# Kernel optimization log

Measured on AMD Instinct MI355X. Metric: run time of the kernel, lower is better.

Reference implementation:

```python
import jax, jax.numpy as jnp
import numpy as np
from jax import lax

GROUPS = 8
EPS = 1e-5


def _gconv(x, W, b, padding):
    y = lax.conv_general_dilated(
        x, W, window_strides=(1, 1), padding=padding,
        feature_group_count=GROUPS,
        dimension_numbers=("NCHW", "OIHW", "NCHW"))
    return y + b[None, :, None, None]


def setup_inputs() -> dict:
    key = jax.random.key(0)
    ks = jax.random.split(key, 9)
    B, C, H, Wd = 2, 256, 48, 48
    cpg = C // GROUPS  # 32 channels per group
    s3 = 1.0 / np.sqrt(cpg * 9)
    s1 = 1.0 / np.sqrt(cpg)
    return {
        "x": jax.random.normal(ks[0], (B, C, H, Wd), jnp.float32),
        "Wq": jax.random.normal(ks[1], (C, cpg, 3, 3), jnp.float32) * s3,
        "bq": jax.random.normal(ks[2], (C,), jnp.float32) * 0.01,
        "Wk": jax.random.normal(ks[3], (C, cpg, 1, 1), jnp.float32) * s1,
        "bk": jax.random.normal(ks[4], (C,), jnp.float32) * 0.01,
        "Wv": jax.random.normal(ks[5], (C, cpg, 1, 1), jnp.float32) * s1,
        "bv": jax.random.normal(ks[6], (C,), jnp.float32) * 0.01,
        "gamma": jnp.ones((C,), jnp.float32),
        "beta": jnp.zeros((C,), jnp.float32),
    }


def reference(x, Wq, bq, Wk, bk, Wv, bv, gamma, beta):
    b, c, h, w = x.shape
    g = GROUPS
    d = c // g  # head dim per group
    hw = h * w

    xq = _gconv(x, Wq, bq, "SAME")    # [b,c,h,w], 3x3 stride1 pad1
    xk = _gconv(x, Wk, bk, "VALID")   # 1x1
    xv = _gconv(x, Wv, bv, "VALID")   # 1x1

    q = xq.reshape(b, g, d, hw)  # k stays [b,g,d,hw]; q,v used as [b,g,hw,d]
    k = xk.reshape(b, g, d, hw)
    v = xv.reshape(b, g, d, hw)

    scale = jnp.asarray(d, x.dtype) ** -0.5
    attn = jnp.einsum("bgdn,bgdm->bgnm", q, k) * scale  # [b,g,hw,hw]
    attn = jax.nn.softmax(attn, axis=-1)
    out = jnp.einsum("bgnm,bgdm->bgdn", attn, v)  # [b,g,d,hw]
    out = out.reshape(b, c, h, w)

    # BatchNorm2d in training mode: biased batch stats over (N,H,W)
    mean = jnp.mean(out, axis=(0, 2, 3), keepdims=True)
    var = jnp.var(out, axis=(0, 2, 3), keepdims=True)
    out = (out - mean) * lax.rsqrt(var + EPS)
    out = out * gamma[None, :, None, None] + beta[None, :, None, None]
    return jax.nn.relu(out)
```

## Files before the change

### kernel.cpp

```cpp
#include <hip/hip_runtime.h>
#include <math.h>

#define BB 2
#define CC 256
#define GG 8
#define DD 32
#define HH 48
#define WW 48
#define HWSZ (HH*WW)
#define NHW (BB*HWSZ)
#define TOT (BB*CC*HWSZ)
#define NBG (BB*GG)
#define KSPLIT 4
#define KSEG (HWSZ/KSPLIT)
#define VTILE 2048
#define ATTN_SCALE (0.17677669529663687f * 1.4426950408889634f)

__device__ __align__(16) short g_q[NBG*HWSZ*DD];
__device__ __align__(16) short g_k[NBG*HWSZ*DD + 2048];
__device__ __align__(16) short g_v[NBG*DD*HWSZ + 2048];
__device__ __align__(16) float g_o[TOT];
__device__ __align__(16) short g_wq[GG*9*2*16*32];
__device__ __align__(16) short g_wk[CC*DD];
__device__ __align__(16) short g_wv[CC*DD];

typedef __attribute__((ext_vector_type(8))) short bf16x8;
typedef __attribute__((ext_vector_type(4))) short s16x4;
typedef __attribute__((ext_vector_type(4))) float f32x4;

__device__ __forceinline__ short f2bf(float f) {
    union { float f; unsigned u; } uf; uf.f = f;
    unsigned r = uf.u + 0x7fff + ((uf.u >> 16) & 1);
    return (short)(r >> 16);
}
__device__ __forceinline__ unsigned cvt_pk_bf16(float lo, float hi) {
    unsigned w;
    asm("v_cvt_pk_bf16_f32 %0, %1, %2" : "=v"(w) : "v"(lo), "v"(hi));
    return w;
}
#if __has_builtin(__builtin_amdgcn_exp2f)
#define EXP2F(x) __builtin_amdgcn_exp2f(x)
#else
#define EXP2F(x) exp2f(x)
#endif

__global__ __launch_bounds__(256) void pack_w(
    const float* __restrict__ Wq, const float* __restrict__ Wk,
    const float* __restrict__ Wv)
{
    int t = blockIdx.x * 256 + threadIdx.x;
    if (t < CC*DD*9) {
        int c = t / 288, r = t % 288, ci = r / 9, tap = r % 9;
        int g = c >> 5, mh = (c >> 4) & 1, l = c & 15;
        g_wq[(((g*9 + tap)*2 + mh)*16 + l)*32 + ci] = f2bf(Wq[t]);
    } else if (t < CC*DD*9 + CC*DD) {
        int i = t - CC*DD*9;
        g_wk[i] = f2bf(Wk[i]);
    } else if (t < CC*DD*9 + 2*CC*DD) {
        int i = t - CC*DD*9 - CC*DD;
        g_wv[i] = f2bf(Wv[i]);
    }
}

__global__ __launch_bounds__(256) void conv_mfma(
    const float* __restrict__ x,
    const float* __restrict__ bq, const float* __restrict__ bk,
    const float* __restrict__ bv)
{
    __shared__ __align__(16) short xt[4*48*40];

    int tid = threadIdx.x;
    int bg = blockIdx.x & 15;
    int pt = blockIdx.x >> 4;
    int p0 = pt * 64;
    int b = bg >> 3, g = bg & 7;
    int r0 = p0 / 48 - 1;
    const float* xb = x + ((size_t)(b*CC + g*DD)) * HWSZ;

    #pragma unroll 4
    for (int i = 0; i < 24; ++i) {
        int cell = tid + i * 256;
        int ci = cell / 192;
        int rc = cell % 192;
        int row = r0 + rc / 48, col = rc % 48;
        float v = (row >= 0 && row < 48) ? xb[(size_t)ci*HWSZ + row*48 + col] : 0.f;
        xt[rc*40 + ci] = f2bf(v);
    }
    __syncthreads();

    int lane = tid & 63, wave = tid >> 6;
    int l15 = lane & 15, lg = lane >> 4;

    bf16x8 aq[9][2], ak[2], av[2];
    const short* wqg = g_wq + g*9*2*16*32;
    #pragma unroll
    for (int tap = 0; tap < 9; ++tap)
        #pragma unroll
        for (int mh = 0; mh < 2; ++mh)
            aq[tap][mh] = *(const bf16x8*)&wqg[((tap*2 + mh)*16 + l15)*32 + lg*8];
    #pragma unroll
    for (int mh = 0; mh < 2; ++mh) {
        ak[mh] = *(const bf16x8*)&g_wk[(g*32 + mh*16 + l15)*32 + lg*8];
        av[mh] = *(const bf16x8*)&g_wv[(g*32 + mh*16 + l15)*32 + lg*8];
    }
    float bqv[2][4], bkv[2][4], bvv[2][4];
    #pragma unroll
    for (int mh = 0; mh < 2; ++mh)
        #pragma unroll
        for (int j = 0; j < 4; ++j) {
            int c = g*32 + mh*16 + lg*4 + j;
            bqv[mh][j] = bq[c]; bkv[mh][j] = bk[c]; bvv[mh][j] = bv[c];
        }

    size_t qkb = (size_t)bg * HWSZ * DD;
    size_t vb  = (size_t)bg * DD * HWSZ;
    const f32x4 zero = {0.f,0.f,0.f,0.f};

    int n = p0 + wave * 16 + l15;
    int y = n / 48, xcol = n % 48;
    int cell = (y - r0) * 48 + xcol;
    f32x4 cq0 = zero, cq1 = zero, ck0 = zero, ck1 = zero, cv0 = zero, cv1 = zero;
    #pragma unroll
    for (int tap = 0; tap < 9; ++tap) {
        int dy = tap / 3 - 1, dx = tap % 3 - 1;
        int xc = xcol + dx;
        bool ok = (unsigned)xc < 48u;
        int idx = ok ? (cell + dy*48 + dx)*40 + lg*8 : lg*8;
        bf16x8 bx = *(const bf16x8*)&xt[idx];
        if (!ok) bx = bf16x8{0,0,0,0,0,0,0,0};
        cq0 = __builtin_amdgcn_mfma_f32_16x16x32_bf16(aq[tap][0], bx, cq0, 0, 0, 0);
        cq1 = __builtin_amdgcn_mfma_f32_16x16x32_bf16(aq[tap][1], bx, cq1, 0, 0, 0);
        if (tap == 4) {
            ck0 = __builtin_amdgcn_mfma_f32_16x16x32_bf16(ak[0], bx, ck0, 0, 0, 0);
            ck1 = __builtin_amdgcn_mfma_f32_16x16x32_bf16(ak[1], bx, ck1, 0, 0, 0);
            cv0 = __builtin_amdgcn_mfma_f32_16x16x32_bf16(av[0], bx, cv0, 0, 0, 0);
            cv1 = __builtin_amdgcn_mfma_f32_16x16x32_bf16(av[1], bx, cv1, 0, 0, 0);
        }
    }
    int tile = n >> 6, key = n & 63;
    #pragma unroll
    for (int mh = 0; mh < 2; ++mh) {
        f32x4 aQ = mh ? cq1 : cq0;
        f32x4 aK = mh ? ck1 : ck0;
        f32x4 aV = mh ? cv1 : cv0;
        s16x4 pq, pk;
        #pragma unroll
        for (int j = 0; j < 4; ++j) {
            pq[j] = f2bf((aQ[j] + bqv[mh][j]) * ATTN_SCALE);
            pk[j] = f2bf(aK[j] + bkv[mh][j]);
        }
        *(s16x4*)&g_q[qkb + (size_t)n*32 + mh*16 + lg*4] = pq;
        *(s16x4*)&g_k[qkb + (size_t)n*32 + mh*16 + lg*4] = pk;
        #pragma unroll
        for (int j = 0; j < 4; ++j)
            g_v[vb + (size_t)tile*VTILE + (mh*16 + lg*4 + j)*64 + key]
                = f2bf(aV[j] + bvv[mh][j]);
    }
}

__global__ __launch_bounds__(256) void attn_mfma()
{
    __shared__ float cmb[KSPLIT][48][34];
    __shared__ float cmbl[KSPLIT][48];

    int tid  = threadIdx.x;
    int lane = tid & 63;
    int ks   = tid >> 6;
    int l15 = lane & 15;
    int lg  = lane >> 4;
    int bg = blockIdx.x & 15;
    int qt = blockIdx.x >> 4;

    const short* qg = g_q + (size_t)bg * HWSZ * DD;
    const short* kg = g_k + (size_t)bg * HWSZ * DD;
    const short* vg = g_v + (size_t)bg * DD * HWSZ;
    int k0 = ks * KSEG;

    bf16x8 aq0 = *(const bf16x8*)&qg[(size_t)(qt*48 + l15)*32 + lg*8];
    bf16x8 aq1 = *(const bf16x8*)&qg[(size_t)(qt*48 + 16 + l15)*32 + lg*8];
    bf16x8 aq2 = *(const bf16x8*)&qg[(size_t)(qt*48 + 32 + l15)*32 + lg*8];

    f32x4 oc00 = {0.f,0.f,0.f,0.f}, oc01 = {0.f,0.f,0.f,0.f};
    f32x4 oc10 = {0.f,0.f,0.f,0.f}, oc11 = {0.f,0.f,0.f,0.f};
    f32x4 oc20 = {0.f,0.f,0.f,0.f}, oc21 = {0.f,0.f,0.f,0.f};
    const f32x4 zero = {0.f,0.f,0.f,0.f};
    float lsum0 = 0.f, lsum1 = 0.f, lsum2 = 0.f;

    int koff = l15*32 + lg*8;
    int voff = l15*64 + lg*8;

    const short* kp = kg + (size_t)k0 * 32;
    const short* vp = vg + (size_t)(ks*9) * VTILE;

    bf16x8 ck[4], cv[4];
    #pragma unroll
    for (int kb = 0; kb < 4; ++kb)
        ck[kb] = *(const bf16x8*)&kp[koff + kb*512];
    #pragma unroll
    for (int h = 0; h < 2; ++h)
        #pragma unroll
        for (int w = 0; w < 2; ++w)
            cv[h*2+w] = *(const bf16x8*)&vp[voff + w*1024 + h*32];

    const short* kq = kp + 2048;
    const short* vq = vp + VTILE;

    for (int t = 0; t < KSEG/64; ++t) {
        bf16x8 nk[4], nv[4];
        #pragma unroll
        for (int kb = 0; kb < 4; ++kb)
            nk[kb] = *(const bf16x8*)&kq[koff + kb*512];
        #pragma unroll
        for (int h = 0; h < 2; ++h)
            #pragma unroll
            for (int w = 0; w < 2; ++w)
                nv[h*2+w] = *(const bf16x8*)&vq[voff + w*1024 + h*32];

        #pragma unroll
        for (int qf = 0; qf < 3; ++qf) {
            bf16x8 aq = qf == 0 ? aq0 : (qf == 1 ? aq1 : aq2);
            f32x4 s[4];
            #pragma unroll
            for (int kb = 0; kb < 4; ++kb)
                s[kb] = __builtin_amdgcn_mfma_f32_16x16x32_bf16(ck[kb], aq, zero, 0, 0, 0);
            unsigned W[4][2];
            float ls = 0.f;
            #pragma unroll
            for (int kb = 0; kb < 4; ++kb) {
                float p0 = EXP2F(s[kb][0]), p1 = EXP2F(s[kb][1]);
                float p2 = EXP2F(s[kb][2]), p3 = EXP2F(s[kb][3]);
                ls += (p0 + p1) + (p2 + p3);
                W[kb][0] = cvt_pk_bf16(p0, p1);
                W[kb][1] = cvt_pk_bf16(p2, p3);
            }
            if (qf == 0) lsum0 += ls; else if (qf == 1) lsum1 += ls; else lsum2 += ls;
            #pragma unroll
            for (int h = 0; h < 2; ++h) {
                unsigned a0 = W[2*h][0], b0 = W[2*h+1][0];
                asm("v_permlane32_swap_b32 %0, %1" : "+v"(a0), "+v"(b0));
                asm("v_permlane16_swap_b32 %0, %1" : "+v"(a0), "+v"(b0));
                unsigned a1 = W[2*h][1], b1 = W[2*h+1][1];
                asm("v_permlane32_swap_b32 %0, %1" : "+v"(a1), "+v"(b1));
                asm("v_permlane16_swap_b32 %0, %1" : "+v"(a1), "+v"(b1));
                union { unsigned u[4]; bf16x8 v; } fr;
                fr.u[0] = a0; fr.u[1] = a1; fr.u[2] = b0; fr.u[3] = b1;
                if (qf == 0) {
                    oc00 = __builtin_amdgcn_mfma_f32_16x16x32_bf16(cv[h*2+0], fr.v, oc00, 0, 0, 0);
                    oc01 = __builtin_amdgcn_mfma_f32_16x16x32_bf16(cv[h*2+1], fr.v, oc01, 0, 0, 0);
                } else if (qf == 1) {
                    oc10 = __builtin_amdgcn_mfma_f32_16x16x32_bf16(cv[h*2+0], fr.v, oc10, 0, 0, 0);
                    oc11 = __builtin_amdgcn_mfma_f32_16x16x32_bf16(cv[h*2+1], fr.v, oc11, 0, 0, 0);
                } else {
                    oc20 = __builtin_amdgcn_mfma_f32_16x16x32_bf16(cv[h*2+0], fr.v, oc20, 0, 0, 0);
                    oc21 = __builtin_amdgcn_mfma_f32_16x16x32_bf16(cv[h*2+1], fr.v, oc21, 0, 0, 0);
                }
            }
        }

        #pragma unroll
        for (int kb = 0; kb < 4; ++kb) ck[kb] = nk[kb];
        #pragma unroll
        for (int i = 0; i < 4; ++i) cv[i] = nv[i];
        kq += 2048;
        vq += VTILE;
    }

    lsum0 += __shfl_xor(lsum0, 16, 64);
    lsum0 += __shfl_xor(lsum0, 32, 64);
    lsum1 += __shfl_xor(lsum1, 16, 64);
    lsum1 += __shfl_xor(lsum1, 32, 64);
    lsum2 += __shfl_xor(lsum2, 16, 64);
    lsum2 += __shfl_xor(lsum2, 32, 64);

    #pragma unroll
    for (int qf = 0; qf < 3; ++qf) {
        f32x4 a = qf == 0 ? oc00 : (qf == 1 ? oc10 : oc20);
        f32x4 b = qf == 0 ? oc01 : (qf == 1 ? oc11 : oc21);
        #pragma unroll
        for (int j = 0; j < 4; ++j) {
            cmb[ks][qf*16 + l15][lg*4 + j]      = a[j];
            cmb[ks][qf*16 + l15][16 + lg*4 + j] = b[j];
        }
    }
    if (lg == 0) {
        cmbl[ks][l15]      = lsum0;
        cmbl[ks][16 + l15] = lsum1;
        cmbl[ks][32 + l15] = lsum2;
    }
    __syncthreads();

    size_t ob = (size_t)bg * DD * HWSZ;
    int n0 = qt * 48;
    for (int i = tid; i < 48*DD; i += 256) {
        int q = i % 48, d = i / 48;
        float num = cmb[0][q][d] + cmb[1][q][d] + cmb[2][q][d] + cmb[3][q][d];
        float den = cmbl[0][q] + cmbl[1][q] + cmbl[2][q] + cmbl[3][q];
        g_o[ob + (size_t)d * HWSZ + n0 + q] = num / den;
    }
}

__global__ __launch_bounds__(256) void bn_relu(
    const float* __restrict__ gamma, const float* __restrict__ beta,
    float* __restrict__ out)
{
    __shared__ float rs[4], rss[4];
    __shared__ float smean, sinv;
    int c = blockIdx.x;
    int tid = threadIdx.x;
    const float* o0 = g_o + (size_t)c * HWSZ;
    const float* o1 = g_o + (size_t)(CC + c) * HWSZ;

    float s = 0.f, ss = 0.f;
    for (int i = tid; i < HWSZ; i += 256) {
        float v0 = o0[i], v1 = o1[i];
        s += v0 + v1;
        ss += v0 * v0 + v1 * v1;
    }
    #pragma unroll
    for (int off = 32; off; off >>= 1) {
        s  += __shfl_down(s, off, 64);
        ss += __shfl_down(ss, off, 64);
    }
    int wid = tid >> 6, lane = tid & 63;
    if (lane == 0) { rs[wid] = s; rss[wid] = ss; }
    __syncthreads();
    if (tid == 0) {
        float ts  = rs[0] + rs[1] + rs[2] + rs[3];
        float tss = rss[0] + rss[1] + rss[2] + rss[3];
        float mean = ts / (float)NHW;
        float var  = tss / (float)NHW - mean * mean;
        smean = mean;
        sinv  = rsqrtf(var + 1e-5f);
    }
    __syncthreads();
    float mean = smean, inv = sinv;
    float ga = gamma[c], be = beta[c];
    float* out0 = out + (size_t)c * HWSZ;
    float* out1 = out + (size_t)(CC + c) * HWSZ;
    for (int i = tid; i < HWSZ; i += 256) {
        float v0 = (o0[i] - mean) * inv * ga + be;
        float v1 = (o1[i] - mean) * inv * ga + be;
        out0[i] = fmaxf(v0, 0.f);
        out1[i] = fmaxf(v1, 0.f);
    }
}

extern "C" void kernel_launch(void* const* d_in, const int* in_sizes, int n_in,
                              void* d_out, int out_size, void* d_ws, size_t ws_size,
                              hipStream_t stream)
{
    const float* x     = (const float*)d_in[0];
    const float* Wq    = (const float*)d_in[1];
    const float* bq    = (const float*)d_in[2];
    const float* Wk    = (const float*)d_in[3];
    const float* bk    = (const float*)d_in[4];
    const float* Wv    = (const float*)d_in[5];
    const float* bv    = (const float*)d_in[6];
    const float* gamma = (const float*)d_in[7];
    const float* beta  = (const float*)d_in[8];
    float* out = (float*)d_out;

    pack_w<<<(CC*DD*9 + 2*CC*DD + 255) / 256, 256, 0, stream>>>(Wq, Wk, Wv);
    conv_mfma<<<NBG * 36, 256, 0, stream>>>(x, bq, bk, bv);
    attn_mfma<<<NBG * 48, 256, 0, stream>>>();
    bn_relu<<<CC, 256, 0, stream>>>(gamma, beta, out);
}
```

Before: 52.91 us.

## Enlarge attention query tile to 64 and fuse BN partial stats into attention epilogue

Each attention block now handles 64 queries instead of 48, giving 576 blocks instead of 768 and reusing each loaded K/V tile across four query fragments instead of three. The attention epilogue also accumulates per-channel sum and sum-of-squares through shared-memory atomics and writes per-block partials. bn_relu then reduces those partials instead of re-reading the whole attention output to compute statistics. The cost is more registers per thread, fewer blocks to spread across the GPU, and LDS atomic contention in the epilogue.

```diff
diff --git a/kernel.cpp b/kernel.cpp
--- a/kernel.cpp
+++ b/kernel.cpp
@@ -14,12 +14,15 @@
 #define KSPLIT 4
 #define KSEG (HWSZ/KSPLIT)
 #define VTILE 2048
+#define NQT 36
 #define ATTN_SCALE (0.17677669529663687f * 1.4426950408889634f)
 
 __device__ __align__(16) short g_q[NBG*HWSZ*DD];
 __device__ __align__(16) short g_k[NBG*HWSZ*DD + 2048];
 __device__ __align__(16) short g_v[NBG*DD*HWSZ + 2048];
 __device__ __align__(16) float g_o[TOT];
+__device__ __align__(16) float g_bsum[NBG*NQT*32];
+__device__ __align__(16) float g_bss[NBG*NQT*32];
 __device__ __align__(16) short g_wq[GG*9*2*16*32];
 __device__ __align__(16) short g_wk[CC*DD];
 __device__ __align__(16) short g_wv[CC*DD];
@@ -158,10 +161,11 @@
     }
 }
 
-__global__ __launch_bounds__(256) void attn_mfma()
-{
-    __shared__ float cmb[KSPLIT][48][34];
-    __shared__ float cmbl[KSPLIT][48];
+__global__ __launch_bounds__(256, 3) void attn_mfma()
+{
+    __shared__ float cmb[KSPLIT][64][34];
+    __shared__ float cmbl[KSPLIT][64];
+    __shared__ float lsm[32], lss[32];
 
     int tid  = threadIdx.x;
     int lane = tid & 63;
@@ -176,15 +180,17 @@
     const short* vg = g_v + (size_t)bg * DD * HWSZ;
     int k0 = ks * KSEG;
 
-    bf16x8 aq0 = *(const bf16x8*)&qg[(size_t)(qt*48 + l15)*32 + lg*8];
-    bf16x8 aq1 = *(const bf16x8*)&qg[(size_t)(qt*48 + 16 + l15)*32 + lg*8];
-    bf16x8 aq2 = *(const bf16x8*)&qg[(size_t)(qt*48 + 32 + l15)*32 + lg*8];
+    bf16x8 aq0 = *(const bf16x8*)&qg[(size_t)(qt*64 + l15)*32 + lg*8];
+    bf16x8 aq1 = *(const bf16x8*)&qg[(size_t)(qt*64 + 16 + l15)*32 + lg*8];
+    bf16x8 aq2 = *(const bf16x8*)&qg[(size_t)(qt*64 + 32 + l15)*32 + lg*8];
+    bf16x8 aq3 = *(const bf16x8*)&qg[(size_t)(qt*64 + 48 + l15)*32 + lg*8];
 
     f32x4 oc00 = {0.f,0.f,0.f,0.f}, oc01 = {0.f,0.f,0.f,0.f};
     f32x4 oc10 = {0.f,0.f,0.f,0.f}, oc11 = {0.f,0.f,0.f,0.f};
     f32x4 oc20 = {0.f,0.f,0.f,0.f}, oc21 = {0.f,0.f,0.f,0.f};
+    f32x4 oc30 = {0.f,0.f,0.f,0.f}, oc31 = {0.f,0.f,0.f,0.f};
     const f32x4 zero = {0.f,0.f,0.f,0.f};
-    float lsum0 = 0.f, lsum1 = 0.f, lsum2 = 0.f;
+    float lsum0 = 0.f, lsum1 = 0.f, lsum2 = 0.f, lsum3 = 0.f;
 
     int koff = l15*32 + lg*8;
     int voff = l15*64 + lg*8;
@@ -217,8 +223,8 @@
                 nv[h*2+w] = *(const bf16x8*)&vq[voff + w*1024 + h*32];
 
         #pragma unroll
-        for (int qf = 0; qf < 3; ++qf) {
-            bf16x8 aq = qf == 0 ? aq0 : (qf == 1 ? aq1 : aq2);
+        for (int qf = 0; qf < 4; ++qf) {
+            bf16x8 aq = qf == 0 ? aq0 : (qf == 1 ? aq1 : (qf == 2 ? aq2 : aq3));
             f32x4 s[4];
             #pragma unroll
             for (int kb = 0; kb < 4; ++kb)
@@ -233,7 +239,8 @@
                 W[kb][0] = cvt_pk_bf16(p0, p1);
                 W[kb][1] = cvt_pk_bf16(p2, p3);
             }
-            if (qf == 0) lsum0 += ls; else if (qf == 1) lsum1 += ls; else lsum2 += ls;
+            if (qf == 0) lsum0 += ls; else if (qf == 1) lsum1 += ls;
+            else if (qf == 2) lsum2 += ls; else lsum3 += ls;
             #pragma unroll
             for (int h = 0; h < 2; ++h) {
                 unsigned a0 = W[2*h][0], b0 = W[2*h+1][0];
@@ -250,9 +257,12 @@
                 } else if (qf == 1) {
                     oc10 = __builtin_amdgcn_mfma_f32_16x16x32_bf16(cv[h*2+0], fr.v, oc10, 0, 0, 0);
                     oc11 = __builtin_amdgcn_mfma_f32_16x16x32_bf16(cv[h*2+1], fr.v, oc11, 0, 0, 0);
-                } else {
+                } else if (qf == 2) {
                     oc20 = __builtin_amdgcn_mfma_f32_16x16x32_bf16(cv[h*2+0], fr.v, oc20, 0, 0, 0);
                     oc21 = __builtin_amdgcn_mfma_f32_16x16x32_bf16(cv[h*2+1], fr.v, oc21, 0, 0, 0);
+                } else {
+                    oc30 = __builtin_amdgcn_mfma_f32_16x16x32_bf16(cv[h*2+0], fr.v, oc30, 0, 0, 0);
+                    oc31 = __builtin_amdgcn_mfma_f32_16x16x32_bf16(cv[h*2+1], fr.v, oc31, 0, 0, 0);
                 }
             }
         }
@@ -271,11 +281,13 @@
     lsum1 += __shfl_xor(lsum1, 32, 64);
     lsum2 += __shfl_xor(lsum2, 16, 64);
     lsum2 += __shfl_xor(lsum2, 32, 64);
-
-    #pragma unroll
-    for (int qf = 0; qf < 3; ++qf) {
-        f32x4 a = qf == 0 ? oc00 : (qf == 1 ? oc10 : oc20);
-        f32x4 b = qf == 0 ? oc01 : (qf == 1 ? oc11 : oc21);
+    lsum3 += __shfl_xor(lsum3, 16, 64);
+    lsum3 += __shfl_xor(lsum3, 32, 64);
+
+    #pragma unroll
+    for (int qf = 0; qf < 4; ++qf) {
+        f32x4 a = qf == 0 ? oc00 : (qf == 1 ? oc10 : (qf == 2 ? oc20 : oc30));
+        f32x4 b = qf == 0 ? oc01 : (qf == 1 ? oc11 : (qf == 2 ? oc21 : oc31));
         #pragma unroll
         for (int j = 0; j < 4; ++j) {
             cmb[ks][qf*16 + l15][lg*4 + j]      = a[j];
@@ -286,16 +298,27 @@
         cmbl[ks][l15]      = lsum0;
         cmbl[ks][16 + l15] = lsum1;
         cmbl[ks][32 + l15] = lsum2;
-    }
+        cmbl[ks][48 + l15] = lsum3;
+    }
+    if (tid < 32) { lsm[tid] = 0.f; lss[tid] = 0.f; }
     __syncthreads();
 
     size_t ob = (size_t)bg * DD * HWSZ;
-    int n0 = qt * 48;
-    for (int i = tid; i < 48*DD; i += 256) {
-        int q = i % 48, d = i / 48;
+    int n0 = qt * 64;
+    for (int i = tid; i < 64*DD; i += 256) {
+        int q = i % 64, d = i / 64;
         float num = cmb[0][q][d] + cmb[1][q][d] + cmb[2][q][d] + cmb[3][q][d];
         float den = cmbl[0][q] + cmbl[1][q] + cmbl[2][q] + cmbl[3][q];
-        g_o[ob + (size_t)d * HWSZ + n0 + q] = num / den;
+        float v = num / den;
+        g_o[ob + (size_t)d * HWSZ + n0 + q] = v;
+        atomicAdd(&lsm[d], v);
+        atomicAdd(&lss[d], v * v);
+    }
+    __syncthreads();
+    if (tid < 32) {
+        int base = (bg * NQT + qt) * 32 + tid;
+        g_bsum[base] = lsm[tid];
+        g_bss[base]  = lss[tid];
     }
 }
 
@@ -307,14 +330,15 @@
     __shared__ float smean, sinv;
     int c = blockIdx.x;
     int tid = threadIdx.x;
-    const float* o0 = g_o + (size_t)c * HWSZ;
-    const float* o1 = g_o + (size_t)(CC + c) * HWSZ;
+    int g = c >> 5, d = c & 31;
 
     float s = 0.f, ss = 0.f;
-    for (int i = tid; i < HWSZ; i += 256) {
-        float v0 = o0[i], v1 = o1[i];
-        s += v0 + v1;
-        ss += v0 * v0 + v1 * v1;
+    for (int i = tid; i < 2*NQT; i += 256) {
+        int bgx = (i < NQT) ? g : 8 + g;
+        int qq  = (i < NQT) ? i : i - NQT;
+        int idx = (bgx * NQT + qq) * 32 + d;
+        s  += g_bsum[idx];
+        ss += g_bss[idx];
     }
     #pragma unroll
     for (int off = 32; off; off >>= 1) {
@@ -335,6 +359,8 @@
     __syncthreads();
     float mean = smean, inv = sinv;
     float ga = gamma[c], be = beta[c];
+    const float* o0 = g_o + (size_t)c * HWSZ;
+    const float* o1 = g_o + (size_t)(CC + c) * HWSZ;
     float* out0 = out + (size_t)c * HWSZ;
     float* out1 = out + (size_t)(CC + c) * HWSZ;
     for (int i = tid; i < HWSZ; i += 256) {
@@ -362,6 +388,6 @@
 
     pack_w<<<(CC*DD*9 + 2*CC*DD + 255) / 256, 256, 0, stream>>>(Wq, Wk, Wv);
     conv_mfma<<<NBG * 36, 256, 0, stream>>>(x, bq, bk, bv);
-    attn_mfma<<<NBG * 48, 256, 0, stream>>>();
+    attn_mfma<<<NBG * NQT, 256, 0, stream>>>();
     bn_relu<<<CC, 256, 0, stream>>>(gamma, beta, out);
 }
```

Result: slower. 69.92 us (+32.2%).
